# Performance work log

Measured on AMD Instinct MI355X. Metric: run time of the kernel, lower is better.

Reference implementation:

```python
import jax, jax.numpy as jnp
import numpy as np

B, T, C = 2, 2048, 1024
N_HEAD = 16
BAND_WIDTH = 256

def setup_inputs() -> dict:
    key = jax.random.key(0)
    ks = jax.random.split(key, 5)
    s = 1.0 / np.sqrt(C)
    return {
        "x": jax.random.normal(ks[0], (B, T, C), dtype=jnp.float32),
        "Wq": jax.random.normal(ks[1], (C, C), dtype=jnp.float32) * s,
        "bq": jnp.zeros((C,), dtype=jnp.float32),
        "Wk": jax.random.normal(ks[2], (C, C), dtype=jnp.float32) * s,
        "bk": jnp.zeros((C,), dtype=jnp.float32),
        "Wv": jax.random.normal(ks[3], (C, C), dtype=jnp.float32) * s,
        "bv": jnp.zeros((C,), dtype=jnp.float32),
        "Wp": jax.random.normal(ks[4], (C, C), dtype=jnp.float32) * s,
        "bp": jnp.zeros((C,), dtype=jnp.float32),
    }

def _band_mask(t):
    # allowed: j <= i (causal) and j >= i - band_width (band)
    i = jnp.arange(t)[:, None]
    j = jnp.arange(t)[None, :]
    return (j <= i) & (j >= i - BAND_WIDTH)

def reference(x, Wq, bq, Wk, bk, Wv, bv, Wp, bp):
    b, t, c = x.shape
    hd = c // N_HEAD
    # projections -> [b, h, t, hd]
    def heads(w, bias):
        y = x @ w.T + bias
        return y.reshape(b, t, N_HEAD, hd).transpose(0, 2, 1, 3)
    q = heads(Wq, bq)
    k = heads(Wk, bk)
    v = heads(Wv, bv)
    scale = 1.0 / np.sqrt(hd)
    att = jnp.einsum('bhqd,bhkd->bhqk', q, k) * scale  # [b,h,t,t]
    mask = _band_mask(t)
    att = jnp.where(mask[None, None], att, -jnp.inf)
    att = jax.nn.softmax(att, axis=-1)
    y = jnp.einsum('bhqk,bhkd->bhqd', att, v)
    y = y.transpose(0, 2, 1, 3).reshape(b, t, c)
    return y @ Wp.T + bp
```

## Files before the change

### kernel.cpp

```cpp
#include <hip/hip_runtime.h>


typedef __attribute__((ext_vector_type(8))) short bf16x8;
typedef __attribute__((ext_vector_type(8))) unsigned short u16x8;
typedef __attribute__((ext_vector_type(4))) float f32x4;

__device__ __forceinline__ float bf2f(unsigned short u) {
  union { unsigned u; float f; } x; x.u = ((unsigned)u) << 16; return x.f;
}
__device__ __forceinline__ unsigned short f2bf(float f) {
  union { float f; unsigned u; } x; x.f = f;
  unsigned r = x.u + 0x7FFFu + ((x.u >> 16) & 1u);
  return (unsigned short)(r >> 16);
}

#define GLOAD_LDS16(g, l)                                                     \
  __builtin_amdgcn_global_load_lds(                                           \
      (__attribute__((address_space(1))) void*)(g),                           \
      (__attribute__((address_space(3))) void*)(l), 16, 0, 0)

__global__ void cvt_all(const float* __restrict__ x, const float* __restrict__ Wq,
                        const float* __restrict__ Wk, const float* __restrict__ Wv,
                        const float* __restrict__ Wp, unsigned short* __restrict__ xb,
                        unsigned short* __restrict__ wqkv,
                        unsigned short* __restrict__ wpb) {
  int i = blockIdx.x * 256 + threadIdx.x;
  const float* src;
  unsigned short* dst;
  int off;
  if (i < 1048576)      { src = x;  dst = xb;             off = i; }
  else if (i < 1310720) { src = Wq; dst = wqkv;           off = i - 1048576; }
  else if (i < 1572864) { src = Wk; dst = wqkv + 1048576; off = i - 1310720; }
  else if (i < 1835008) { src = Wv; dst = wqkv + 2097152; off = i - 1572864; }
  else                  { src = Wp; dst = wpb;            off = i - 1835008; }
  float4 v = ((const float4*)src)[off];
  ushort4 o;
  o.x = f2bf(v.x); o.y = f2bf(v.y); o.z = f2bf(v.z); o.w = f2bf(v.w);
  ((ushort4*)dst)[off] = o;
}

template <int MODE>
__global__ __launch_bounds__(256) void gemm_bt(
    const unsigned short* __restrict__ A, const unsigned short* __restrict__ Wall,
    const float* __restrict__ b0, const float* __restrict__ b1,
    const float* __restrict__ b2, void* __restrict__ outp) {
  constexpr int K = 1024;
  __shared__ __align__(16) unsigned short As[128 * 32];
  __shared__ __align__(16) unsigned short Bs[128 * 32];
  int tid = threadIdx.x;
  int m0 = blockIdx.x * 128;
  int n0;
  const unsigned short* W;
  const float* bias;
  void* out;
  int proj = 0;
  if (MODE == 1) {
    proj = blockIdx.y >> 3;
    n0 = (blockIdx.y & 7) * 128;
    W = Wall + (size_t)proj * (K * 1024);
    bias = (proj == 0) ? b0 : ((proj == 1) ? b1 : b2);
    out = (void*)((unsigned short*)outp + (size_t)proj * 4194304);
  } else {
    n0 = blockIdx.y * 128;
    W = Wall;
    bias = b0;
    out = outp;
  }
  int w = tid >> 6, lane = tid & 63;
  int wm = (w >> 1) * 64, wn = (w & 1) * 64;
  int lm = lane & 15, quad = lane >> 4;

  f32x4 acc[4][4];
#pragma unroll
  for (int mi = 0; mi < 4; ++mi)
#pragma unroll
    for (int ni = 0; ni < 4; ++ni) acc[mi][ni] = (f32x4){0.f, 0.f, 0.f, 0.f};

  int o0 = tid * 16, o1 = o0 + 4096;
  int r0 = o0 >> 6, cb0 = o0 & 63;
  int r1 = o1 >> 6, cb1 = o1 & 63;
  const char* a0 = (const char*)A + (size_t)(m0 + r0) * (K * 2) + cb0;
  const char* a1 = (const char*)A + (size_t)(m0 + r1) * (K * 2) + cb1;
  const char* w0 = (const char*)W + (size_t)(n0 + r0) * (K * 2) + cb0;
  const char* w1 = (const char*)W + (size_t)(n0 + r1) * (K * 2) + cb1;
  char* lA = (char*)As;
  char* lB = (char*)Bs;

  for (int k0 = 0; k0 < K; k0 += 32) {
    GLOAD_LDS16(a0 + k0 * 2, lA + o0);
    GLOAD_LDS16(a1 + k0 * 2, lA + o1);
    GLOAD_LDS16(w0 + k0 * 2, lB + o0);
    GLOAD_LDS16(w1 + k0 * 2, lB + o1);
    __syncthreads();
    bf16x8 af[4], bfv[4];
#pragma unroll
    for (int mi = 0; mi < 4; ++mi)
      af[mi] = *(const bf16x8*)(As + (wm + mi * 16 + lm) * 32 + quad * 8);
#pragma unroll
    for (int ni = 0; ni < 4; ++ni)
      bfv[ni] = *(const bf16x8*)(Bs + (wn + ni * 16 + lm) * 32 + quad * 8);
#pragma unroll
    for (int mi = 0; mi < 4; ++mi)
#pragma unroll
      for (int ni = 0; ni < 4; ++ni)
        acc[mi][ni] = __builtin_amdgcn_mfma_f32_16x16x32_bf16(
            af[mi], bfv[ni], acc[mi][ni], 0, 0, 0);
    __syncthreads();
  }
#pragma unroll
  for (int mi = 0; mi < 4; ++mi) {
#pragma unroll
    for (int ni = 0; ni < 4; ++ni) {
      int gn = n0 + wn + ni * 16 + lm;
      float bv = bias[gn];
#pragma unroll
      for (int r = 0; r < 4; ++r) {
        int gm = m0 + wm + mi * 16 + quad * 4 + r;
        float val = acc[mi][ni][r] + bv;
        if (MODE == 0) {
          ((float*)out)[(size_t)gm * 1024 + gn] = val;
        } else {
          int bb = gm >> 11, tt = gm & 2047;
          int hh = gn >> 6, dd = gn & 63;
          size_t idx;
          if (proj == 2)
            idx = (((size_t)bb * 16 + hh) * 64 + dd) * 2048 + tt;
          else
            idx = (((size_t)bb * 16 + hh) * 2048 + tt) * 64 + dd;
          ((unsigned short*)out)[idx] = f2bf(val);
        }
      }
    }
  }
}

__global__ __launch_bounds__(256) void attn_band_mfma(
    const unsigned short* __restrict__ qb, const unsigned short* __restrict__ kb,
    const unsigned short* __restrict__ vtg, unsigned short* __restrict__ yb) {
  __shared__ __align__(16) unsigned short Ps[64 * 72];
  int bid = blockIdx.x;
  int qt = bid & 31, h = (bid >> 5) & 15, b = bid >> 9;
  int q0b = qt * 64;
  int tid = threadIdx.x;
  int w = tid >> 6, lane = tid & 63;
  int m = lane & 15, quad = lane >> 4;
  int wq = w * 16;
  int tq0 = q0b + wq;
  size_t hb = ((size_t)(b * 16 + h)) * (2048 * 64);
  size_t vhb = ((size_t)(b * 16 + h)) * (64 * 2048);

  const unsigned short* qrow = qb + hb + (size_t)(tq0 + m) * 64;
  bf16x8 af0 = *(const bf16x8*)(qrow + quad * 8);
  bf16x8 af1 = *(const bf16x8*)(qrow + 32 + quad * 8);

  f32x4 oacc[4];
#pragma unroll
  for (int di = 0; di < 4; ++di) oacc[di] = (f32x4){0.f, 0.f, 0.f, 0.f};
  float lpart[4] = {0.f, 0.f, 0.f, 0.f};

  int jlo = q0b - 256;
  if (jlo < 0) jlo = 0;
  for (int c0 = jlo; c0 <= q0b; c0 += 64) {
    f32x4 sacc[4];
#pragma unroll
    for (int ni = 0; ni < 4; ++ni) sacc[ni] = (f32x4){0.f, 0.f, 0.f, 0.f};
    const unsigned short* kbase = kb + hb + (size_t)c0 * 64;
#pragma unroll
    for (int ks = 0; ks < 2; ++ks) {
      bf16x8 a = ks ? af1 : af0;
#pragma unroll
      for (int ni = 0; ni < 4; ++ni) {
        bf16x8 bfr =
            *(const bf16x8*)(kbase + (size_t)(ni * 16 + m) * 64 + ks * 32 + quad * 8);
        sacc[ni] = __builtin_amdgcn_mfma_f32_16x16x32_bf16(a, bfr, sacc[ni], 0, 0, 0);
      }
    }
#pragma unroll
    for (int ni = 0; ni < 4; ++ni) {
      int j = c0 + ni * 16 + m;
#pragma unroll
      for (int r = 0; r < 4; ++r) {
        int t = tq0 + quad * 4 + r;
        float e = __expf(sacc[ni][r] * 0.125f);
        e = ((unsigned)(t - j) <= 256u) ? e : 0.f;
        lpart[r] += e;
        Ps[(wq + quad * 4 + r) * 72 + ni * 16 + m] = f2bf(e);
      }
    }
    const unsigned short* vbase = vtg + vhb + c0;
#pragma unroll
    for (int ks = 0; ks < 2; ++ks) {
      bf16x8 a = *(const bf16x8*)(Ps + (wq + m) * 72 + ks * 32 + quad * 8);
#pragma unroll
      for (int di = 0; di < 4; ++di) {
        bf16x8 bfr =
            *(const bf16x8*)(vbase + (size_t)(di * 16 + m) * 2048 + ks * 32 + quad * 8);
        oacc[di] = __builtin_amdgcn_mfma_f32_16x16x32_bf16(a, bfr, oacc[di], 0, 0, 0);
      }
    }
  }
#pragma unroll
  for (int mask = 1; mask <= 8; mask <<= 1)
#pragma unroll
    for (int r = 0; r < 4; ++r) lpart[r] += __shfl_xor(lpart[r], mask, 64);
  float inv[4];
#pragma unroll
  for (int r = 0; r < 4; ++r) inv[r] = 1.f / lpart[r];
#pragma unroll
  for (int di = 0; di < 4; ++di)
#pragma unroll
    for (int r = 0; r < 4; ++r)
      Ps[(wq + quad * 4 + r) * 72 + di * 16 + m] = f2bf(oacc[di][r] * inv[r]);
  size_t orow = (size_t)b * 2048 + tq0;
#pragma unroll
  for (int v2 = 0; v2 < 2; ++v2) {
    int v = v2 * 64 + lane;
    int q = v >> 3, dg = v & 7;
    u16x8 val = *(const u16x8*)(Ps + (wq + q) * 72 + dg * 8);
    *(u16x8*)(yb + (orow + q) * 1024 + h * 64 + dg * 8) = val;
  }
}

extern "C" void kernel_launch(void* const* d_in, const int* in_sizes, int n_in,
                              void* d_out, int out_size, void* d_ws,
                              size_t ws_size, hipStream_t stream) {
  const float* x  = (const float*)d_in[0];
  const float* Wq = (const float*)d_in[1];
  const float* bq = (const float*)d_in[2];
  const float* Wk = (const float*)d_in[3];
  const float* bk = (const float*)d_in[4];
  const float* Wv = (const float*)d_in[5];
  const float* bv = (const float*)d_in[6];
  const float* Wp = (const float*)d_in[7];
  const float* bp = (const float*)d_in[8];
  float* out = (float*)d_out;

  char* ws = (char*)d_ws;
  unsigned short* xb   = (unsigned short*)(ws);
  unsigned short* wqkv = (unsigned short*)(ws + (8ull << 20));
  unsigned short* wpb  = (unsigned short*)(ws + (14ull << 20));
  unsigned short* qkv  = (unsigned short*)(ws + (16ull << 20));
  unsigned short* yb   = (unsigned short*)(ws + (40ull << 20));

  cvt_all<<<8192, 256, 0, stream>>>(x, Wq, Wk, Wv, Wp, xb, wqkv, wpb);
  gemm_bt<1><<<dim3(32, 24), 256, 0, stream>>>(xb, wqkv, bq, bk, bv, (void*)qkv);
  attn_band_mfma<<<1024, 256, 0, stream>>>(qkv, qkv + 4194304ull,
                                           qkv + 8388608ull, yb);
  gemm_bt<0><<<dim3(32, 8), 256, 0, stream>>>(yb, wpb, bp, nullptr, nullptr,
                                              (void*)out);
}
```

Baseline: 189.5 us.

## Double the GEMM K-step per barrier and stage QKV epilogue through LDS

The GEMM main loop now loads two 32-wide K slices per iteration into four LDS buffers, which halves the number of barrier pairs per tile. The QKV epilogue writes each warp's bf16 64x64 tile into LDS, transposed for V, and then stores it with 16-byte vector writes instead of scattered 2-byte stores. This targets barrier overhead and uncoalesced global writes. It doubles LDS use per block, which may lower occupancy.

```diff
diff --git a/kernel.cpp b/kernel.cpp
--- a/kernel.cpp
+++ b/kernel.cpp
@@ -45,8 +45,7 @@
     const float* __restrict__ b0, const float* __restrict__ b1,
     const float* __restrict__ b2, void* __restrict__ outp) {
   constexpr int K = 1024;
-  __shared__ __align__(16) unsigned short As[128 * 32];
-  __shared__ __align__(16) unsigned short Bs[128 * 32];
+  __shared__ __align__(16) unsigned short L[4][128 * 32];
   int tid = threadIdx.x;
   int m0 = blockIdx.x * 128;
   int n0;
@@ -83,52 +82,91 @@
   const char* a1 = (const char*)A + (size_t)(m0 + r1) * (K * 2) + cb1;
   const char* w0 = (const char*)W + (size_t)(n0 + r0) * (K * 2) + cb0;
   const char* w1 = (const char*)W + (size_t)(n0 + r1) * (K * 2) + cb1;
-  char* lA = (char*)As;
-  char* lB = (char*)Bs;
-
-  for (int k0 = 0; k0 < K; k0 += 32) {
-    GLOAD_LDS16(a0 + k0 * 2, lA + o0);
-    GLOAD_LDS16(a1 + k0 * 2, lA + o1);
-    GLOAD_LDS16(w0 + k0 * 2, lB + o0);
-    GLOAD_LDS16(w1 + k0 * 2, lB + o1);
+  char* lA0 = (char*)L[0];
+  char* lA1 = (char*)L[1];
+  char* lB0 = (char*)L[2];
+  char* lB1 = (char*)L[3];
+
+  for (int k0 = 0; k0 < K; k0 += 64) {
+    int kb = k0 * 2;
+    GLOAD_LDS16(a0 + kb, lA0 + o0);
+    GLOAD_LDS16(a1 + kb, lA0 + o1);
+    GLOAD_LDS16(a0 + kb + 64, lA1 + o0);
+    GLOAD_LDS16(a1 + kb + 64, lA1 + o1);
+    GLOAD_LDS16(w0 + kb, lB0 + o0);
+    GLOAD_LDS16(w1 + kb, lB0 + o1);
+    GLOAD_LDS16(w0 + kb + 64, lB1 + o0);
+    GLOAD_LDS16(w1 + kb + 64, lB1 + o1);
     __syncthreads();
-    bf16x8 af[4], bfv[4];
-#pragma unroll
-    for (int mi = 0; mi < 4; ++mi)
-      af[mi] = *(const bf16x8*)(As + (wm + mi * 16 + lm) * 32 + quad * 8);
-#pragma unroll
-    for (int ni = 0; ni < 4; ++ni)
-      bfv[ni] = *(const bf16x8*)(Bs + (wn + ni * 16 + lm) * 32 + quad * 8);
-#pragma unroll
-    for (int mi = 0; mi < 4; ++mi)
+#pragma unroll
+    for (int s = 0; s < 2; ++s) {
+      const unsigned short* As = L[s];
+      const unsigned short* Bs = L[2 + s];
+      bf16x8 af[4], bfv[4];
+#pragma unroll
+      for (int mi = 0; mi < 4; ++mi)
+        af[mi] = *(const bf16x8*)(As + (wm + mi * 16 + lm) * 32 + quad * 8);
 #pragma unroll
       for (int ni = 0; ni < 4; ++ni)
-        acc[mi][ni] = __builtin_amdgcn_mfma_f32_16x16x32_bf16(
-            af[mi], bfv[ni], acc[mi][ni], 0, 0, 0);
+        bfv[ni] = *(const bf16x8*)(Bs + (wn + ni * 16 + lm) * 32 + quad * 8);
+#pragma unroll
+      for (int mi = 0; mi < 4; ++mi)
+#pragma unroll
+        for (int ni = 0; ni < 4; ++ni)
+          acc[mi][ni] = __builtin_amdgcn_mfma_f32_16x16x32_bf16(
+              af[mi], bfv[ni], acc[mi][ni], 0, 0, 0);
+    }
     __syncthreads();
   }
-#pragma unroll
-  for (int mi = 0; mi < 4; ++mi) {
-#pragma unroll
-    for (int ni = 0; ni < 4; ++ni) {
-      int gn = n0 + wn + ni * 16 + lm;
-      float bv = bias[gn];
-#pragma unroll
-      for (int r = 0; r < 4; ++r) {
-        int gm = m0 + wm + mi * 16 + quad * 4 + r;
-        float val = acc[mi][ni][r] + bv;
-        if (MODE == 0) {
-          ((float*)out)[(size_t)gm * 1024 + gn] = val;
-        } else {
-          int bb = gm >> 11, tt = gm & 2047;
-          int hh = gn >> 6, dd = gn & 63;
-          size_t idx;
-          if (proj == 2)
-            idx = (((size_t)bb * 16 + hh) * 64 + dd) * 2048 + tt;
-          else
-            idx = (((size_t)bb * 16 + hh) * 2048 + tt) * 64 + dd;
-          ((unsigned short*)out)[idx] = f2bf(val);
+  if (MODE == 0) {
+#pragma unroll
+    for (int mi = 0; mi < 4; ++mi) {
+#pragma unroll
+      for (int ni = 0; ni < 4; ++ni) {
+        int gn = n0 + wn + ni * 16 + lm;
+        float bv = bias[gn];
+#pragma unroll
+        for (int r = 0; r < 4; ++r) {
+          int gm = m0 + wm + mi * 16 + quad * 4 + r;
+          ((float*)out)[(size_t)gm * 1024 + gn] = acc[mi][ni][r] + bv;
         }
+      }
+    }
+  } else {
+    unsigned short* R = &L[0][0] + w * 4096;
+    int bb = (m0 + wm) >> 11, tt0 = (m0 + wm) & 2047;
+    int hh = (n0 + wn) >> 6;
+#pragma unroll
+    for (int mi = 0; mi < 4; ++mi) {
+#pragma unroll
+      for (int ni = 0; ni < 4; ++ni) {
+        float bv = bias[(size_t)(n0 + wn + ni * 16 + lm)];
+#pragma unroll
+        for (int r = 0; r < 4; ++r) {
+          unsigned short val = f2bf(acc[mi][ni][r] + bv);
+          int ml = mi * 16 + quad * 4 + r;
+          int nl = ni * 16 + lm;
+          if (proj == 2) R[nl * 64 + ml] = val;
+          else           R[ml * 64 + nl] = val;
+        }
+      }
+    }
+    if (proj == 2) {
+      unsigned short* vb =
+          (unsigned short*)out + (((size_t)bb * 16 + hh) * 64) * 2048 + tt0;
+#pragma unroll
+      for (int it = 0; it < 8; ++it) {
+        int v = it * 64 + lane;
+        int r = v >> 3, c8 = v & 7;
+        *(u16x8*)(vb + (size_t)r * 2048 + c8 * 8) = *(const u16x8*)(R + v * 8);
+      }
+    } else {
+      unsigned short* qb =
+          (unsigned short*)out + (((size_t)bb * 16 + hh) * 2048 + tt0) * 64;
+#pragma unroll
+      for (int it = 0; it < 8; ++it) {
+        int v = it * 64 + lane;
+        *(u16x8*)(qb + v * 8) = *(const u16x8*)(R + v * 8);
       }
     }
   }
```

Result: slower. 195.1 us (+2.9%).
